# Kernel tuning notes

Hardware: AMD Instinct MI355X
Metric: run time of the kernel (lower is better)

## Reference

```python
import jax, jax.numpy as jnp
import numpy as np
import math

N, S, D, BF, K, NT, NL = 4096, 64, 256, 24, 8, 64, 4096

def setup_inputs() -> dict:
    key = jax.random.key(0)
    ks = jax.random.split(key, 20)
    inp = {
        "values": jax.random.normal(ks[0], (N, S), dtype=jnp.float32),
        "kinds": jax.random.randint(ks[1], (N, S), 0, K, dtype=jnp.int32),
        "mask": jax.random.randint(ks[2], (N, S), 0, 2, dtype=jnp.int32),
        "prim_type": jax.random.randint(ks[3], (N,), 0, NT, dtype=jnp.int32),
        "layer_id": jax.random.randint(ks[4], (N,), 0, NL, dtype=jnp.int32),
        "meta": jax.random.normal(ks[5], (N, 4), dtype=jnp.float32),
        # frozen Fourier projection (sigma=8)
        "B_ff": jax.random.normal(ks[6], (1, BF), dtype=jnp.float32) * 8.0,
        # embeddings (N(0,1) like nn.Embedding default)
        "kind_emb_w": jax.random.normal(ks[7], (K, D), dtype=jnp.float32),
        "type_emb_w": jax.random.normal(ks[8], (NT, D), dtype=jnp.float32),
        "layer_emb_w": jax.random.normal(ks[9], (NL, D), dtype=jnp.float32),
        # per-kind MLPs: 2B -> D -> D
        "mlp_w1": jax.random.normal(ks[10], (K, 2 * BF, D), dtype=jnp.float32) / np.sqrt(2 * BF),
        "mlp_b1": jnp.zeros((K, D), dtype=jnp.float32),
        "mlp_w2": jax.random.normal(ks[11], (K, D, D), dtype=jnp.float32) / np.sqrt(D),
        "mlp_b2": jnp.zeros((K, D), dtype=jnp.float32),
        # fuse: 3D -> D -> D
        "fuse_w1": jax.random.normal(ks[12], (3 * D, D), dtype=jnp.float32) / np.sqrt(3 * D),
        "fuse_b1": jnp.zeros((D,), dtype=jnp.float32),
        "fuse_w2": jax.random.normal(ks[13], (D, D), dtype=jnp.float32) / np.sqrt(D),
        "fuse_b2": jnp.zeros((D,), dtype=jnp.float32),
        # meta_lin: 4 -> D
        "meta_w": jax.random.normal(ks[14], (4, D), dtype=jnp.float32) / 2.0,
        "meta_b": jnp.zeros((D,), dtype=jnp.float32),
    }
    return inp

def _gelu(x):
    return jax.nn.gelu(x, approximate=False)  # torch nn.GELU default = exact erf

def reference(values, kinds, mask, prim_type, layer_id, meta, B_ff,
              kind_emb_w, type_emb_w, layer_emb_w,
              mlp_w1, mlp_b1, mlp_w2, mlp_b2,
              fuse_w1, fuse_b1, fuse_w2, fuse_b2, meta_w, meta_b):
    n, s = values.shape
    d = kind_emb_w.shape[1]
    k_kinds = kind_emb_w.shape[0]
    # Fourier features over all N*S scalar slots -> [NS, 2B]
    y = (2.0 * math.pi) * values.reshape(-1, 1) @ B_ff
    ff = jnp.concatenate([jnp.sin(y), jnp.cos(y)], axis=-1)
    kf = kinds.reshape(-1)
    # kind-routed per-kind MLP (dispatch/combine expressed as masked combine)
    out = jnp.zeros((n * s, d), dtype=values.dtype)
    for k in range(k_kinds):
        h = _gelu(ff @ mlp_w1[k] + mlp_b1[k]) @ mlp_w2[k] + mlp_b2[k]
        out = jnp.where((kf == k)[:, None], h, out)
    h_slots = out.reshape(n, s, d) + kind_emb_w[kinds]
    m = mask.astype(values.dtype)
    h_slots = h_slots * m[..., None]
    denom = jnp.clip(m.sum(axis=1, keepdims=True), 1.0)  # [N,1]
    h_num = h_slots.sum(axis=1) / denom  # masked mean pooling -> [N,D]
    h = jnp.concatenate([h_num, type_emb_w[prim_type], layer_emb_w[layer_id]], axis=-1)
    fused = _gelu(h @ fuse_w1 + fuse_b1) @ fuse_w2 + fuse_b2
    return fused + meta @ meta_w + meta_b
```

## Files before the change

kernel.cpp:

```cpp
#include <hip/hip_runtime.h>
#include <math.h>


#define W2F_HI   0
#define W2F_LO   524288
#define W1F_HI   1048576
#define W1F_LO   1179648
#define FW1F_HI  1310720
#define FW1F_LO  1507328
#define FW2F_HI  1703936
#define FW2F_LO  1769472
#define POOL_BYTE  3670016ull
#define CNT_BYTE   37224448ull
#define DEN_BYTE   37355520ull

typedef __attribute__((ext_vector_type(8))) short frag;
typedef __attribute__((ext_vector_type(4))) float f32x4;

__device__ __forceinline__ unsigned short f2bf_rn(float x) {
    unsigned int u = __float_as_uint(x);
    unsigned int r = (u + 0x7fffu + ((u >> 16) & 1u)) >> 16;
    return (unsigned short)r;
}
__device__ __forceinline__ float bf2f(unsigned short h) {
    return __uint_as_float(((unsigned int)h) << 16);
}
__device__ __forceinline__ void split_bf(float x, unsigned short& h, unsigned short& l) {
    unsigned short hh = f2bf_rn(x);
    h = hh;
    l = f2bf_rn(x - bf2f(hh));
}

__device__ __forceinline__ float gelu_fast(float x) {
    float u = fabsf(x) * 0.7071067811865476f;
    float t = __builtin_amdgcn_rcpf(fmaf(0.3275911f, u, 1.0f));
    float p = fmaf(fmaf(fmaf(fmaf(1.061405429f, t, -1.453152027f), t,
                             1.421413741f), t, -0.284496736f), t, 0.254829592f) * t;
    float e = __expf(-u * u);
    float er = fmaf(-p, e, 1.0f);
    er = copysignf(er, x);
    return 0.5f * x * (1.0f + er);
}

__global__ __launch_bounds__(512) void prep_kernel(
    const float* __restrict__ w1, const float* __restrict__ w2,
    const float* __restrict__ fw1, const float* __restrict__ fw2,
    short* __restrict__ ws)
{
    int tid = blockIdx.x * 512 + threadIdx.x;
    int fid = tid >> 6, ln = tid & 63;
    if (fid >= 1792) return;
    int lr = ln & 15, kq = ln >> 4;
    float v[8];
    int dhi, dlo, dsto;
    if (fid < 1024) {
        int k = fid >> 7, kst = (fid >> 4) & 7, nt = fid & 15;
        int col = nt * 16 + lr;
        #pragma unroll
        for (int b = 0; b < 8; ++b) {
            int kg = kst * 32 + kq * 8 + b;
            v[b] = w2[(k * 256 + kg) * 256 + col];
        }
        dsto = fid * 512 + ln * 8; dhi = W2F_HI; dlo = W2F_LO;
    } else if (fid < 1280) {
        int f = fid - 1024;
        int k = f >> 5, kst = (f >> 4) & 1, nt = f & 15;
        int col = nt * 16 + lr;
        #pragma unroll
        for (int b = 0; b < 8; ++b) {
            int kg = kst * 32 + kq * 8 + b;
            v[b] = (kg < 48) ? w1[(k * 48 + kg) * 256 + col] : 0.0f;
        }
        dsto = f * 512 + ln * 8; dhi = W1F_HI; dlo = W1F_LO;
    } else if (fid < 1664) {
        int f = fid - 1280;
        int kst = f >> 4, nt = f & 15;
        int col = nt * 16 + lr;
        #pragma unroll
        for (int b = 0; b < 8; ++b) {
            int kg = kst * 32 + kq * 8 + b;
            v[b] = fw1[kg * 256 + col];
        }
        dsto = f * 512 + ln * 8; dhi = FW1F_HI; dlo = FW1F_LO;
    } else {
        int f = fid - 1664;
        int kst = f >> 4, nt = f & 15;
        int col = nt * 16 + lr;
        #pragma unroll
        for (int b = 0; b < 8; ++b) {
            int kg = kst * 32 + kq * 8 + b;
            v[b] = fw2[kg * 256 + col];
        }
        dsto = f * 512 + ln * 8; dhi = FW2F_HI; dlo = FW2F_LO;
    }
    union { unsigned short u[8]; frag f; } hu, lu;
    #pragma unroll
    for (int b = 0; b < 8; ++b) split_bf(v[b], hu.u[b], lu.u[b]);
    *(frag*)(ws + dhi + dsto) = hu.f;
    *(frag*)(ws + dlo + dsto) = lu.f;
}

template<int MODE>
__global__ __launch_bounds__(256, 4) void mlpfused_kernel(
    const float* __restrict__ values, const int* __restrict__ kinds,
    const int* __restrict__ mask, const short* __restrict__ wsf,
    const float* __restrict__ B_ff, const float* __restrict__ b1,
    float* __restrict__ poolf, float* __restrict__ cntf,
    float* __restrict__ denf)
{
    __shared__ float vals_ls[1024];
    __shared__ unsigned char knd_ls[1024], msk_ls[1024];
    __shared__ unsigned short list[1088];
    __shared__ int len_s;
    __shared__ float pool[16 * 257];
    __shared__ float Bs_ls[24], b1_ls[256];

    const int t = threadIdx.x, blk = blockIdx.x;
    const int q = blk >> 3, k = blk & 7;
    const int wv = t >> 6, ln = t & 63, lr16 = ln & 15, kq = ln >> 4;
    const int gbase = q * 1024;

    const short* w1f_hi = wsf + W1F_HI;
    const short* w1f_lo = wsf + W1F_LO;

    #pragma unroll
    for (int i = 0; i < 4; ++i) {
        int p = t + i * 256;
        vals_ls[p] = values[gbase + p];
        knd_ls[p]  = (unsigned char)kinds[gbase + p];
        msk_ls[p]  = (unsigned char)mask[gbase + p];
    }
    if (t < 24) Bs_ls[t] = B_ff[t];
    b1_ls[t] = b1[k * 256 + t];
    for (int i = t; i < 16 * 257; i += 256) pool[i] = 0.0f;
    __syncthreads();

    #pragma unroll
    for (int j = 0; j < 4; ++j) {
        int r = wv * 4 + j;
        int kd = knd_ls[r * 64 + ln], mk = msk_ls[r * 64 + ln];
        unsigned long long balk = __ballot(mk && (kd == k));
        unsigned long long balm = __ballot(mk != 0);
        if (ln == 0) {
            cntf[(q * 16 + r) * 8 + k] = (float)__popcll(balk);
            if (k == 0) {
                int tot = __popcll(balm);
                denf[q * 16 + r] = 1.0f / (float)(tot > 0 ? tot : 1);
            }
        }
    }

    if (t < 64) {
        const unsigned long long below = (1ull << ln) - 1ull;
        int fill = 0;
        for (int c = 0; c < 16; ++c) {
            int p = c * 64 + ln;
            int kd = knd_ls[p], mk = msk_ls[p];
            unsigned long long bal = __ballot(mk && (kd == k));
            if (mk && (kd == k)) list[fill + __popcll(bal & below)] = (unsigned short)p;
            fill += __popcll(bal);
        }
        if (ln == 0) len_s = fill;
        int pad = (fill + 63) & ~63;
        for (int i = fill + ln; i < pad; i += 64) list[i] = 0xFFFFu;
    }
    __syncthreads();

    const int ntl = (len_s + 15) >> 4;

    for (int m = wv; m < ntl; m += 4) {
        int slot = list[m * 16 + lr16];
        float v = vals_ls[slot & 1023];
        v = (slot == 0xFFFFu) ? 0.0f : v;

        frag ah[2], al[2];
        #pragma unroll
        for (int kst = 0; kst < 2; ++kst) {
            union { unsigned short u[8]; frag f; } hu, lu;
            int jb0 = kst * 32 + kq * 8;
            #pragma unroll
            for (int b = 0; b < 8; ++b) {
                int jb = jb0 + b;
                float sv;
                if (jb < 48) {
                    int jm = (jb < 24) ? jb : jb - 24;
                    float cadd = (jb < 24) ? 0.0f : 0.25f;
                    float rev = __builtin_amdgcn_fractf(fmaf(v, Bs_ls[jm], cadd));
                    sv = __builtin_amdgcn_sinf(rev);
                } else {
                    sv = 0.0f;
                }
                split_bf(sv, hu.u[b], lu.u[b]);
            }
            ah[kst] = hu.f; al[kst] = lu.f;
        }

        if (MODE == 3) {
            asm volatile("" :: "v"((int)ah[0][0]), "v"((int)ah[1][0]),
                              "v"((int)al[0][0]), "v"((int)al[1][0]));
            continue;
        }

        int e4[4];
        #pragma unroll
        for (int r = 0; r < 4; ++r) {
            int sl = list[m * 16 + kq * 4 + r];
            e4[r] = (sl == 0xFFFFu) ? -1 : (sl >> 6);
        }

        #pragma unroll 4
        for (int nt = 0; nt < 16; ++nt) {
            int o0 = ((k * 2 + 0) * 16 + nt) * 512 + ln * 8;
            int o1 = ((k * 2 + 1) * 16 + nt) * 512 + ln * 8;
            frag bh0 = *(const frag*)(w1f_hi + o0);
            frag bl0 = *(const frag*)(w1f_lo + o0);
            frag bh1 = *(const frag*)(w1f_hi + o1);
            frag bl1 = *(const frag*)(w1f_lo + o1);
            f32x4 acc = (f32x4)0.0f;
            acc = __builtin_amdgcn_mfma_f32_16x16x32_bf16(ah[0], bh0, acc, 0, 0, 0);
            acc = __builtin_amdgcn_mfma_f32_16x16x32_bf16(al[0], bh0, acc, 0, 0, 0);
            acc = __builtin_amdgcn_mfma_f32_16x16x32_bf16(ah[0], bl0, acc, 0, 0, 0);
            acc = __builtin_amdgcn_mfma_f32_16x16x32_bf16(ah[1], bh1, acc, 0, 0, 0);
            acc = __builtin_amdgcn_mfma_f32_16x16x32_bf16(al[1], bh1, acc, 0, 0, 0);
            acc = __builtin_amdgcn_mfma_f32_16x16x32_bf16(ah[1], bl1, acc, 0, 0, 0);
            float b1v = b1_ls[nt * 16 + lr16];
            #pragma unroll
            for (int r = 0; r < 4; ++r) {
                if (e4[r] >= 0) {
                    float g = gelu_fast(acc[r] + b1v);
                    atomicAdd(&pool[e4[r] * 257 + nt * 16 + lr16], g);
                }
            }
        }
    }
    __syncthreads();

    for (int i = t; i < 16 * 256; i += 256) {
        int r = i >> 8, c = i & 255;
        poolf[((size_t)k * 4096 + q * 16 + r) * 256 + c] = pool[r * 257 + c];
    }
}

__global__ __launch_bounds__(512) void fuse_kernel(
    const short* __restrict__ ws, const float* __restrict__ poolf,
    const float* __restrict__ cntf, const float* __restrict__ denf,
    const int* __restrict__ pt, const int* __restrict__ lid,
    const float* __restrict__ meta, const float* __restrict__ type_emb,
    const float* __restrict__ layer_emb, const float* __restrict__ b2,
    const float* __restrict__ kind_emb, const float* __restrict__ fb1,
    const float* __restrict__ fb2, const float* __restrict__ meta_w,
    const float* __restrict__ meta_b, float* __restrict__ out)
{
    __shared__ __align__(16) short Af[2][2][4096];
    __shared__ __align__(16) float hz[4096];
    __shared__ float cnt_s[128], den_s[16], meta_s[64];
    __shared__ int pt_s[16], lid_s[16];

    const short* w2f_hi  = ws + W2F_HI;
    const short* w2f_lo  = ws + W2F_LO;
    const short* fw1f_hi = ws + FW1F_HI;
    const short* fw1f_lo = ws + FW1F_LO;
    const short* fw2f_hi = ws + FW2F_HI;
    const short* fw2f_lo = ws + FW2F_LO;

    const int t = threadIdx.x, blk = blockIdx.x, rb = blk * 16;
    const int wv = t >> 6, ln = t & 63, lr16 = ln & 15, kq = ln >> 4;

    if (t < 16) { pt_s[t] = pt[rb + t]; lid_s[t] = lid[rb + t]; den_s[t] = denf[rb + t]; }
    else if (t < 144) cnt_s[t - 16] = cntf[rb * 8 + (t - 16)];
    else if (t < 208) meta_s[t - 144] = meta[rb * 4 + (t - 144)];

    const int sr = t >> 5, sg = t & 31;
    const int skst = sg >> 2, skq = sg & 3;
    const int slane = skq * 16 + sr;
    const int sdst = slane * 64 + ((skst ^ (sr & 7)) << 3);

    auto stage = [&](int k, int buf) {
        const float* src = poolf + ((size_t)k * 4096 + rb + sr) * 256 + sg * 8;
        f32x4 u0 = *(const f32x4*)src;
        f32x4 u1 = *(const f32x4*)(src + 4);
        union { unsigned short u[8]; frag f; } hu, lu;
        #pragma unroll
        for (int b = 0; b < 4; ++b) {
            split_bf(u0[b], hu.u[b], lu.u[b]);
            split_bf(u1[b], hu.u[b + 4], lu.u[b + 4]);
        }
        *(frag*)&Af[buf][0][sdst] = hu.f;
        *(frag*)&Af[buf][1][sdst] = lu.f;
    };

    stage(0, 0);
    __syncthreads();

    f32x4 acc[2];
    acc[0] = (f32x4)0.0f; acc[1] = (f32x4)0.0f;

    for (int k = 0; k < 8; ++k) {
        const int buf = k & 1;
        if (k < 7) stage(k + 1, buf ^ 1);
        #pragma unroll 2
        for (int kst = 0; kst < 8; ++kst) {
            int ao = ln * 64 + ((kst ^ (ln & 7)) << 3);
            frag ah = *(const frag*)&Af[buf][0][ao];
            frag al = *(const frag*)&Af[buf][1][ao];
            #pragma unroll
            for (int n = 0; n < 2; ++n) {
                size_t bo = (((size_t)k * 8 + kst) * 16 + (wv * 2 + n)) * 512 + ln * 8;
                frag bh = *(const frag*)(w2f_hi + bo);
                frag bl = *(const frag*)(w2f_lo + bo);
                acc[n] = __builtin_amdgcn_mfma_f32_16x16x32_bf16(ah, bh, acc[n], 0, 0, 0);
                acc[n] = __builtin_amdgcn_mfma_f32_16x16x32_bf16(al, bh, acc[n], 0, 0, 0);
                acc[n] = __builtin_amdgcn_mfma_f32_16x16x32_bf16(ah, bl, acc[n], 0, 0, 0);
            }
        }
        __syncthreads();
    }

    #pragma unroll
    for (int n = 0; n < 2; ++n) {
        int col = (wv * 2 + n) * 16 + lr16;
        float bks[8];
        #pragma unroll
        for (int k = 0; k < 8; ++k) bks[k] = b2[k * 256 + col] + kind_emb[k * 256 + col];
        #pragma unroll
        for (int r = 0; r < 4; ++r) {
            int row = kq * 4 + r;
            float hv = acc[n][r];
            #pragma unroll
            for (int k = 0; k < 8; ++k) hv = fmaf(cnt_s[row * 8 + k], bks[k], hv);
            hv *= den_s[row];
            hz[row * 256 + ((((col >> 2) ^ (row & 7)) << 2) | (col & 3))] = hv;
        }
    }
    __syncthreads();

    f32x4 az[2];
    az[0] = (f32x4)0.0f; az[1] = (f32x4)0.0f;

    for (int kst = 0; kst < 24; ++kst) {
        const int row = lr16;
        union { unsigned short u[8]; frag f; } hu, lu;
        if (kst < 8) {
            int c0 = kst * 8 + kq * 2;
            f32x4 u0 = *(const f32x4*)&hz[row * 256 + ((c0 ^ (row & 7)) << 2)];
            f32x4 u1 = *(const f32x4*)&hz[row * 256 + (((c0 + 1) ^ (row & 7)) << 2)];
            #pragma unroll
            for (int b = 0; b < 4; ++b) {
                split_bf(u0[b], hu.u[b], lu.u[b]);
                split_bf(u1[b], hu.u[b + 4], lu.u[b + 4]);
            }
        } else {
            const float* eb = (kst < 16) ? type_emb : layer_emb;
            const int* ids = (kst < 16) ? pt_s : lid_s;
            int ko = (kst & 7) * 32 + kq * 8;
            const float* sp = eb + (size_t)ids[row] * 256 + ko;
            f32x4 u0 = *(const f32x4*)sp;
            f32x4 u1 = *(const f32x4*)(sp + 4);
            #pragma unroll
            for (int b = 0; b < 4; ++b) {
                split_bf(u0[b], hu.u[b], lu.u[b]);
                split_bf(u1[b], hu.u[b + 4], lu.u[b + 4]);
            }
        }
        frag ah = hu.f, al = lu.f;
        #pragma unroll
        for (int n = 0; n < 2; ++n) {
            size_t bo = ((size_t)kst * 16 + (wv * 2 + n)) * 512 + ln * 8;
            frag bh = *(const frag*)(fw1f_hi + bo);
            frag bl = *(const frag*)(fw1f_lo + bo);
            az[n] = __builtin_amdgcn_mfma_f32_16x16x32_bf16(ah, bh, az[n], 0, 0, 0);
            az[n] = __builtin_amdgcn_mfma_f32_16x16x32_bf16(al, bh, az[n], 0, 0, 0);
            az[n] = __builtin_amdgcn_mfma_f32_16x16x32_bf16(ah, bl, az[n], 0, 0, 0);
        }
    }
    __syncthreads();

    #pragma unroll
    for (int n = 0; n < 2; ++n) {
        int col = (wv * 2 + n) * 16 + lr16;
        float fb1v = fb1[col];
        #pragma unroll
        for (int r = 0; r < 4; ++r) {
            int row = kq * 4 + r;
            float z = gelu_fast(az[n][r] + fb1v);
            hz[row * 256 + ((((col >> 2) ^ (row & 7)) << 2) | (col & 3))] = z;
        }
    }
    __syncthreads();

    f32x4 ao2[2];
    ao2[0] = (f32x4)0.0f; ao2[1] = (f32x4)0.0f;

    for (int kst = 0; kst < 8; ++kst) {
        const int row = lr16;
        int c0 = kst * 8 + kq * 2;
        f32x4 u0 = *(const f32x4*)&hz[row * 256 + ((c0 ^ (row & 7)) << 2)];
        f32x4 u1 = *(const f32x4*)&hz[row * 256 + (((c0 + 1) ^ (row & 7)) << 2)];
        union { unsigned short u[8]; frag f; } hu, lu;
        #pragma unroll
        for (int b = 0; b < 4; ++b) {
            split_bf(u0[b], hu.u[b], lu.u[b]);
            split_bf(u1[b], hu.u[b + 4], lu.u[b + 4]);
        }
        frag ah = hu.f, al = lu.f;
        #pragma unroll
        for (int n = 0; n < 2; ++n) {
            size_t bo = ((size_t)kst * 16 + (wv * 2 + n)) * 512 + ln * 8;
            frag bh = *(const frag*)(fw2f_hi + bo);
            frag bl = *(const frag*)(fw2f_lo + bo);
            ao2[n] = __builtin_amdgcn_mfma_f32_16x16x32_bf16(ah, bh, ao2[n], 0, 0, 0);
            ao2[n] = __builtin_amdgcn_mfma_f32_16x16x32_bf16(al, bh, ao2[n], 0, 0, 0);
            ao2[n] = __builtin_amdgcn_mfma_f32_16x16x32_bf16(ah, bl, ao2[n], 0, 0, 0);
        }
    }

    #pragma unroll
    for (int n = 0; n < 2; ++n) {
        int col = (wv * 2 + n) * 16 + lr16;
        float ob = fb2[col] + meta_b[col];
        float mw0 = meta_w[col], mw1 = meta_w[256 + col];
        float mw2 = meta_w[512 + col], mw3 = meta_w[768 + col];
        #pragma unroll
        for (int r = 0; r < 4; ++r) {
            int row = kq * 4 + r;
            float o = ao2[n][r] + ob;
            o = fmaf(meta_s[row * 4 + 0], mw0, o);
            o = fmaf(meta_s[row * 4 + 1], mw1, o);
            o = fmaf(meta_s[row * 4 + 2], mw2, o);
            o = fmaf(meta_s[row * 4 + 3], mw3, o);
            out[(size_t)(rb + row) * 256 + col] = o;
        }
    }
}

extern "C" void kernel_launch(void* const* d_in, const int* in_sizes, int n_in,
                              void* d_out, int out_size, void* d_ws, size_t ws_size,
                              hipStream_t stream) {
    const float* values    = (const float*)d_in[0];
    const int*   kinds     = (const int*)d_in[1];
    const int*   mask      = (const int*)d_in[2];
    const int*   prim_type = (const int*)d_in[3];
    const int*   layer_id  = (const int*)d_in[4];
    const float* meta      = (const float*)d_in[5];
    const float* B_ff      = (const float*)d_in[6];
    const float* kind_emb  = (const float*)d_in[7];
    const float* type_emb  = (const float*)d_in[8];
    const float* layer_emb = (const float*)d_in[9];
    const float* mlp_w1    = (const float*)d_in[10];
    const float* mlp_b1    = (const float*)d_in[11];
    const float* mlp_w2    = (const float*)d_in[12];
    const float* mlp_b2    = (const float*)d_in[13];
    const float* fuse_w1   = (const float*)d_in[14];
    const float* fuse_b1   = (const float*)d_in[15];
    const float* fuse_w2   = (const float*)d_in[16];
    const float* fuse_b2   = (const float*)d_in[17];
    const float* meta_w    = (const float*)d_in[18];
    const float* meta_b    = (const float*)d_in[19];

    short* ws    = (short*)d_ws;
    float* poolf = (float*)((char*)d_ws + POOL_BYTE);
    float* cntf  = (float*)((char*)d_ws + CNT_BYTE);
    float* denf  = (float*)((char*)d_ws + DEN_BYTE);
    float* out   = (float*)d_out;

    prep_kernel<<<224, 512, 0, stream>>>(mlp_w1, mlp_w2, fuse_w1, fuse_w2, ws);
    mlpfused_kernel<3><<<2048, 256, 0, stream>>>(values, kinds, mask, ws, B_ff,
                                                 mlp_b1, poolf, cntf, denf);
    mlpfused_kernel<0><<<2048, 256, 0, stream>>>(values, kinds, mask, ws, B_ff,
                                                 mlp_b1, poolf, cntf, denf);
    fuse_kernel<<<256, 512, 0, stream>>>(ws, poolf, cntf, denf, prim_type, layer_id,
                                         meta, type_emb, layer_emb, mlp_b2, kind_emb,
                                         fuse_b1, fuse_b2, meta_w, meta_b, out);
}
```

Before: 306.7 us.

## Fuse per-kind MLP and fuse stage into one kernel with LDS-resident pools

Merges the per-kind first-layer MLP kernel and the fuse kernel into a single 256-block kernel. Each block now handles 16 rows across all 8 kinds, building per-kind chunk lists and keeping all eight 16x256 pools in shared memory, so the global pool, count and denominator round trip is gone. It also drops the extra MODE=3 warm-up launch, which repeated the Fourier feature work. In exchange, occupancy falls to one 512-thread block per CU with large LDS use, and only 256 blocks run instead of 2048, which may leave GPU parallelism underused.

Result: faster. 258.4 us (-15.8%).

```diff
diff --git a/kernel.cpp b/kernel.cpp
--- a/kernel.cpp
+++ b/kernel.cpp
@@ -10,9 +10,8 @@
 #define FW1F_LO  1507328
 #define FW2F_HI  1703936
 #define FW2F_LO  1769472
-#define POOL_BYTE  3670016ull
-#define CNT_BYTE   37224448ull
-#define DEN_BYTE   37355520ull
+
+#define PSTR 260
 
 typedef __attribute__((ext_vector_type(8))) short frag;
 typedef __attribute__((ext_vector_type(4))) float f32x4;
@@ -100,78 +99,136 @@
     *(frag*)(ws + dlo + dsto) = lu.f;
 }
 
-template<int MODE>
-__global__ __launch_bounds__(256, 4) void mlpfused_kernel(
+__global__ __launch_bounds__(512, 1) void mono_kernel(
     const float* __restrict__ values, const int* __restrict__ kinds,
-    const int* __restrict__ mask, const short* __restrict__ wsf,
-    const float* __restrict__ B_ff, const float* __restrict__ b1,
-    float* __restrict__ poolf, float* __restrict__ cntf,
-    float* __restrict__ denf)
+    const int* __restrict__ mask, const float* __restrict__ B_ff,
+    const float* __restrict__ b1, const short* __restrict__ wsf,
+    const int* __restrict__ pt, const int* __restrict__ lid,
+    const float* __restrict__ meta, const float* __restrict__ type_emb,
+    const float* __restrict__ layer_emb, const float* __restrict__ b2,
+    const float* __restrict__ kind_emb, const float* __restrict__ fb1,
+    const float* __restrict__ fb2, const float* __restrict__ meta_w,
+    const float* __restrict__ meta_b, float* __restrict__ out)
 {
+    __shared__ __align__(16) float pool_ls[8 * 16 * PSTR];
     __shared__ float vals_ls[1024];
     __shared__ unsigned char knd_ls[1024], msk_ls[1024];
-    __shared__ unsigned short list[1088];
-    __shared__ int len_s;
-    __shared__ float pool[16 * 257];
-    __shared__ float Bs_ls[24], b1_ls[256];
+    __shared__ unsigned short list[1152];
+    __shared__ short chunk_kind[80], chunk_base[80];
+    __shared__ int nch_s;
+    __shared__ float b1_ls[2048];
+    __shared__ float Bs_ls[24];
+    __shared__ float cnt_ls[128], den_ls[16], meta_ls[64];
+    __shared__ int pt_ls[16], lid_ls[16];
 
     const int t = threadIdx.x, blk = blockIdx.x;
-    const int q = blk >> 3, k = blk & 7;
     const int wv = t >> 6, ln = t & 63, lr16 = ln & 15, kq = ln >> 4;
-    const int gbase = q * 1024;
-
-    const short* w1f_hi = wsf + W1F_HI;
-    const short* w1f_lo = wsf + W1F_LO;
-
-    #pragma unroll
-    for (int i = 0; i < 4; ++i) {
-        int p = t + i * 256;
+    const int gbase = blk * 1024, rb = blk * 16;
+
+    const short* w1f_hi  = wsf + W1F_HI;
+    const short* w1f_lo  = wsf + W1F_LO;
+    const short* w2f_hi  = wsf + W2F_HI;
+    const short* w2f_lo  = wsf + W2F_LO;
+    const short* fw1f_hi = wsf + FW1F_HI;
+    const short* fw1f_lo = wsf + FW1F_LO;
+    const short* fw2f_hi = wsf + FW2F_HI;
+    const short* fw2f_lo = wsf + FW2F_LO;
+
+    #pragma unroll
+    for (int i = 0; i < 2; ++i) {
+        int p = t + i * 512;
         vals_ls[p] = values[gbase + p];
         knd_ls[p]  = (unsigned char)kinds[gbase + p];
         msk_ls[p]  = (unsigned char)mask[gbase + p];
     }
+    #pragma unroll
+    for (int i = 0; i < 4; ++i) b1_ls[t + i * 512] = b1[t + i * 512];
     if (t < 24) Bs_ls[t] = B_ff[t];
-    b1_ls[t] = b1[k * 256 + t];
-    for (int i = t; i < 16 * 257; i += 256) pool[i] = 0.0f;
-    __syncthreads();
-
-    #pragma unroll
-    for (int j = 0; j < 4; ++j) {
-        int r = wv * 4 + j;
+    if (t >= 32 && t < 48) { pt_ls[t - 32] = pt[rb + t - 32]; lid_ls[t - 32] = lid[rb + t - 32]; }
+    if (t >= 64 && t < 128) meta_ls[t - 64] = meta[rb * 4 + (t - 64)];
+    for (int i = t; i < 8 * 16 * PSTR; i += 512) pool_ls[i] = 0.0f;
+    __syncthreads();
+
+    #pragma unroll
+    for (int j = 0; j < 2; ++j) {
+        int r = wv * 2 + j;
         int kd = knd_ls[r * 64 + ln], mk = msk_ls[r * 64 + ln];
-        unsigned long long balk = __ballot(mk && (kd == k));
         unsigned long long balm = __ballot(mk != 0);
+        int myc = 0;
+        #pragma unroll
+        for (int k = 0; k < 8; ++k) {
+            unsigned long long bal = __ballot(mk && (kd == k));
+            int c = __popcll(bal);
+            myc = (ln == k) ? c : myc;
+        }
+        if (ln < 8) cnt_ls[r * 8 + ln] = (float)myc;
         if (ln == 0) {
-            cntf[(q * 16 + r) * 8 + k] = (float)__popcll(balk);
-            if (k == 0) {
-                int tot = __popcll(balm);
-                denf[q * 16 + r] = 1.0f / (float)(tot > 0 ? tot : 1);
-            }
+            int tot = __popcll(balm);
+            den_ls[r] = 1.0f / (float)(tot > 0 ? tot : 1);
         }
     }
 
     if (t < 64) {
-        const unsigned long long below = (1ull << ln) - 1ull;
-        int fill = 0;
+        int cnts[8];
+        #pragma unroll
+        for (int k = 0; k < 8; ++k) cnts[k] = 0;
         for (int c = 0; c < 16; ++c) {
-            int p = c * 64 + ln;
+            int p = c * 64 + t;
             int kd = knd_ls[p], mk = msk_ls[p];
-            unsigned long long bal = __ballot(mk && (kd == k));
-            if (mk && (kd == k)) list[fill + __popcll(bal & below)] = (unsigned short)p;
-            fill += __popcll(bal);
-        }
-        if (ln == 0) len_s = fill;
-        int pad = (fill + 63) & ~63;
-        for (int i = fill + ln; i < pad; i += 64) list[i] = 0xFFFFu;
-    }
-    __syncthreads();
-
-    const int ntl = (len_s + 15) >> 4;
-
-    for (int m = wv; m < ntl; m += 4) {
-        int slot = list[m * 16 + lr16];
+            #pragma unroll
+            for (int k = 0; k < 8; ++k) {
+                unsigned long long bal = __ballot(mk && (kd == k));
+                cnts[k] += __popcll(bal);
+            }
+        }
+        int offk[8], run = 0;
+        #pragma unroll
+        for (int k = 0; k < 8; ++k) { offk[k] = run; run += (cnts[k] + 15) & ~15; }
+        int fillk[8];
+        #pragma unroll
+        for (int k = 0; k < 8; ++k) fillk[k] = 0;
+        const unsigned long long below = (1ull << t) - 1ull;
+        for (int c = 0; c < 16; ++c) {
+            int p = c * 64 + t;
+            int kd = knd_ls[p], mk = msk_ls[p];
+            #pragma unroll
+            for (int k = 0; k < 8; ++k) {
+                unsigned long long bal = __ballot(mk && (kd == k));
+                if (mk && (kd == k)) {
+                    int rank = __popcll(bal & below);
+                    list[offk[k] + fillk[k] + rank] = (unsigned short)p;
+                }
+                fillk[k] += __popcll(bal);
+            }
+        }
+        #pragma unroll
+        for (int k = 0; k < 8; ++k) {
+            int padded = (cnts[k] + 15) & ~15;
+            for (int i = cnts[k] + t; i < padded; i += 64) list[offk[k] + i] = 0xFFFFu;
+        }
+        if (t == 0) {
+            int ci = 0;
+            #pragma unroll
+            for (int k = 0; k < 8; ++k) {
+                int nk = (cnts[k] + 15) >> 4;
+                for (int j = 0; j < nk; ++j) {
+                    chunk_kind[ci] = (short)k;
+                    chunk_base[ci] = (short)(offk[k] + j * 16);
+                    ++ci;
+                }
+            }
+            nch_s = ci;
+        }
+    }
+    __syncthreads();
+
+    const int nch = nch_s;
+    for (int m = wv; m < nch; m += 8) {
+        const int k = (int)chunk_kind[m];
+        const int cb = (int)chunk_base[m];
+        int slot = list[cb + lr16];
         float v = vals_ls[slot & 1023];
-        v = (slot == 0xFFFFu) ? 0.0f : v;
+        v = (slot == 0xFFFF) ? 0.0f : v;
 
         frag ah[2], al[2];
         #pragma unroll
@@ -195,17 +252,11 @@
             ah[kst] = hu.f; al[kst] = lu.f;
         }
 
-        if (MODE == 3) {
-            asm volatile("" :: "v"((int)ah[0][0]), "v"((int)ah[1][0]),
-                              "v"((int)al[0][0]), "v"((int)al[1][0]));
-            continue;
-        }
-
         int e4[4];
         #pragma unroll
         for (int r = 0; r < 4; ++r) {
-            int sl = list[m * 16 + kq * 4 + r];
-            e4[r] = (sl == 0xFFFFu) ? -1 : (sl >> 6);
+            int sl = list[cb + kq * 4 + r];
+            e4[r] = (sl == 0xFFFF) ? -1 : ((sl >> 6) & 15);
         }
 
         #pragma unroll 4
@@ -223,89 +274,37 @@
             acc = __builtin_amdgcn_mfma_f32_16x16x32_bf16(ah[1], bh1, acc, 0, 0, 0);
             acc = __builtin_amdgcn_mfma_f32_16x16x32_bf16(al[1], bh1, acc, 0, 0, 0);
             acc = __builtin_amdgcn_mfma_f32_16x16x32_bf16(ah[1], bl1, acc, 0, 0, 0);
-            float b1v = b1_ls[nt * 16 + lr16];
+            float b1v = b1_ls[k * 256 + nt * 16 + lr16];
             #pragma unroll
             for (int r = 0; r < 4; ++r) {
                 if (e4[r] >= 0) {
                     float g = gelu_fast(acc[r] + b1v);
-                    atomicAdd(&pool[e4[r] * 257 + nt * 16 + lr16], g);
+                    atomicAdd(&pool_ls[(k * 16 + e4[r]) * PSTR + nt * 16 + lr16], g);
                 }
             }
         }
     }
-    __syncthreads();
-
-    for (int i = t; i < 16 * 256; i += 256) {
-        int r = i >> 8, c = i & 255;
-        poolf[((size_t)k * 4096 + q * 16 + r) * 256 + c] = pool[r * 257 + c];
-    }
-}
-
-__global__ __launch_bounds__(512) void fuse_kernel(
-    const short* __restrict__ ws, const float* __restrict__ poolf,
-    const float* __restrict__ cntf, const float* __restrict__ denf,
-    const int* __restrict__ pt, const int* __restrict__ lid,
-    const float* __restrict__ meta, const float* __restrict__ type_emb,
-    const float* __restrict__ layer_emb, const float* __restrict__ b2,
-    const float* __restrict__ kind_emb, const float* __restrict__ fb1,
-    const float* __restrict__ fb2, const float* __restrict__ meta_w,
-    const float* __restrict__ meta_b, float* __restrict__ out)
-{
-    __shared__ __align__(16) short Af[2][2][4096];
-    __shared__ __align__(16) float hz[4096];
-    __shared__ float cnt_s[128], den_s[16], meta_s[64];
-    __shared__ int pt_s[16], lid_s[16];
-
-    const short* w2f_hi  = ws + W2F_HI;
-    const short* w2f_lo  = ws + W2F_LO;
-    const short* fw1f_hi = ws + FW1F_HI;
-    const short* fw1f_lo = ws + FW1F_LO;
-    const short* fw2f_hi = ws + FW2F_HI;
-    const short* fw2f_lo = ws + FW2F_LO;
-
-    const int t = threadIdx.x, blk = blockIdx.x, rb = blk * 16;
-    const int wv = t >> 6, ln = t & 63, lr16 = ln & 15, kq = ln >> 4;
-
-    if (t < 16) { pt_s[t] = pt[rb + t]; lid_s[t] = lid[rb + t]; den_s[t] = denf[rb + t]; }
-    else if (t < 144) cnt_s[t - 16] = cntf[rb * 8 + (t - 16)];
-    else if (t < 208) meta_s[t - 144] = meta[rb * 4 + (t - 144)];
-
-    const int sr = t >> 5, sg = t & 31;
-    const int skst = sg >> 2, skq = sg & 3;
-    const int slane = skq * 16 + sr;
-    const int sdst = slane * 64 + ((skst ^ (sr & 7)) << 3);
-
-    auto stage = [&](int k, int buf) {
-        const float* src = poolf + ((size_t)k * 4096 + rb + sr) * 256 + sg * 8;
-        f32x4 u0 = *(const f32x4*)src;
-        f32x4 u1 = *(const f32x4*)(src + 4);
-        union { unsigned short u[8]; frag f; } hu, lu;
-        #pragma unroll
-        for (int b = 0; b < 4; ++b) {
-            split_bf(u0[b], hu.u[b], lu.u[b]);
-            split_bf(u1[b], hu.u[b + 4], lu.u[b + 4]);
-        }
-        *(frag*)&Af[buf][0][sdst] = hu.f;
-        *(frag*)&Af[buf][1][sdst] = lu.f;
-    };
-
-    stage(0, 0);
     __syncthreads();
 
     f32x4 acc[2];
     acc[0] = (f32x4)0.0f; acc[1] = (f32x4)0.0f;
 
     for (int k = 0; k < 8; ++k) {
-        const int buf = k & 1;
-        if (k < 7) stage(k + 1, buf ^ 1);
         #pragma unroll 2
         for (int kst = 0; kst < 8; ++kst) {
-            int ao = ln * 64 + ((kst ^ (ln & 7)) << 3);
-            frag ah = *(const frag*)&Af[buf][0][ao];
-            frag al = *(const frag*)&Af[buf][1][ao];
+            const float* pp = &pool_ls[(k * 16 + lr16) * PSTR + kst * 32 + kq * 8];
+            f32x4 u0 = *(const f32x4*)pp;
+            f32x4 u1 = *(const f32x4*)(pp + 4);
+            union { unsigned short u[8]; frag f; } hu, lu;
+            #pragma unroll
+            for (int b = 0; b < 4; ++b) {
+                split_bf(u0[b], hu.u[b], lu.u[b]);
+                split_bf(u1[b], hu.u[b + 4], lu.u[b + 4]);
+            }
+            frag ah = hu.f, al = lu.f;
             #pragma unroll
             for (int n = 0; n < 2; ++n) {
-                size_t bo = (((size_t)k * 8 + kst) * 16 + (wv * 2 + n)) * 512 + ln * 8;
+                int bo = ((k * 8 + kst) * 16 + (wv * 2 + n)) * 512 + ln * 8;
                 frag bh = *(const frag*)(w2f_hi + bo);
                 frag bl = *(const frag*)(w2f_lo + bo);
                 acc[n] = __builtin_amdgcn_mfma_f32_16x16x32_bf16(ah, bh, acc[n], 0, 0, 0);
@@ -313,8 +312,10 @@
                 acc[n] = __builtin_amdgcn_mfma_f32_16x16x32_bf16(ah, bl, acc[n], 0, 0, 0);
             }
         }
-        __syncthreads();
-    }
+    }
+    __syncthreads();
+
+    float* hz = pool_ls;
 
     #pragma unroll
     for (int n = 0; n < 2; ++n) {
@@ -327,8 +328,8 @@
             int row = kq * 4 + r;
             float hv = acc[n][r];
             #pragma unroll
-            for (int k = 0; k < 8; ++k) hv = fmaf(cnt_s[row * 8 + k], bks[k], hv);
-            hv *= den_s[row];
+            for (int k = 0; k < 8; ++k) hv = fmaf(cnt_ls[row * 8 + k], bks[k], hv);
+            hv *= den_ls[row];
             hz[row * 256 + ((((col >> 2) ^ (row & 7)) << 2) | (col & 3))] = hv;
         }
     }
@@ -351,7 +352,7 @@
             }
         } else {
             const float* eb = (kst < 16) ? type_emb : layer_emb;
-            const int* ids = (kst < 16) ? pt_s : lid_s;
+            const int* ids = (kst < 16) ? pt_ls : lid_ls;
             int ko = (kst & 7) * 32 + kq * 8;
             const float* sp = eb + (size_t)ids[row] * 256 + ko;
             f32x4 u0 = *(const f32x4*)sp;
@@ -365,7 +366,7 @@
         frag ah = hu.f, al = lu.f;
         #pragma unroll
         for (int n = 0; n < 2; ++n) {
-            size_t bo = ((size_t)kst * 16 + (wv * 2 + n)) * 512 + ln * 8;
+            int bo = (kst * 16 + (wv * 2 + n)) * 512 + ln * 8;
             frag bh = *(const frag*)(fw1f_hi + bo);
             frag bl = *(const frag*)(fw1f_lo + bo);
             az[n] = __builtin_amdgcn_mfma_f32_16x16x32_bf16(ah, bh, az[n], 0, 0, 0);
@@ -405,7 +406,7 @@
         frag ah = hu.f, al = lu.f;
         #pragma unroll
         for (int n = 0; n < 2; ++n) {
-            size_t bo = ((size_t)kst * 16 + (wv * 2 + n)) * 512 + ln * 8;
+            int bo = (kst * 16 + (wv * 2 + n)) * 512 + ln * 8;
             frag bh = *(const frag*)(fw2f_hi + bo);
             frag bl = *(const frag*)(fw2f_lo + bo);
             ao2[n] = __builtin_amdgcn_mfma_f32_16x16x32_bf16(ah, bh, ao2[n], 0, 0, 0);
@@ -424,10 +425,10 @@
         for (int r = 0; r < 4; ++r) {
             int row = kq * 4 + r;
             float o = ao2[n][r] + ob;
-            o = fmaf(meta_s[row * 4 + 0], mw0, o);
-            o = fmaf(meta_s[row * 4 + 1], mw1, o);
-            o = fmaf(meta_s[row * 4 + 2], mw2, o);
-            o = fmaf(meta_s[row * 4 + 3], mw3, o);
+            o = fmaf(meta_ls[row * 4 + 0], mw0, o);
+            o = fmaf(meta_ls[row * 4 + 1], mw1, o);
+            o = fmaf(meta_ls[row * 4 + 2], mw2, o);
+            o = fmaf(meta_ls[row * 4 + 3], mw3, o);
             out[(size_t)(rb + row) * 256 + col] = o;
         }
     }
@@ -457,18 +458,12 @@
     const float* meta_w    = (const float*)d_in[18];
     const float* meta_b    = (const float*)d_in[19];
 
-    short* ws    = (short*)d_ws;
-    float* poolf = (float*)((char*)d_ws + POOL_BYTE);
-    float* cntf  = (float*)((char*)d_ws + CNT_BYTE);
-    float* denf  = (float*)((char*)d_ws + DEN_BYTE);
-    float* out   = (float*)d_out;
+    short* ws  = (short*)d_ws;
+    float* out = (float*)d_out;
 
     prep_kernel<<<224, 512, 0, stream>>>(mlp_w1, mlp_w2, fuse_w1, fuse_w2, ws);
-    mlpfused_kernel<3><<<2048, 256, 0, stream>>>(values, kinds, mask, ws, B_ff,
-                                                 mlp_b1, poolf, cntf, denf);
-    mlpfused_kernel<0><<<2048, 256, 0, stream>>>(values, kinds, mask, ws, B_ff,
-                                                 mlp_b1, poolf, cntf, denf);
-    fuse_kernel<<<256, 512, 0, stream>>>(ws, poolf, cntf, denf, prim_type, layer_id,
-                                         meta, type_emb, layer_emb, mlp_b2, kind_emb,
-                                         fuse_b1, fuse_b2, meta_w, meta_b, out);
-}
+    mono_kernel<<<256, 512, 0, stream>>>(values, kinds, mask, B_ff, mlp_b1, ws,
+                                         prim_type, layer_id, meta, type_emb,
+                                         layer_emb, mlp_b2, kind_emb, fuse_b1,
+                                         fuse_b2, meta_w, meta_b, out);
+}
```
